# Optimization experiments

Hardware: AMD Instinct MI355X
Metric: run time of the kernel (lower is better)

The kernel has to match this reference:

```python
import jax, jax.numpy as jnp
import numpy as np

N, K, D = 32768, 8192, 64

def setup_inputs() -> dict:
    key = jax.random.key(0)
    kx, kc = jax.random.split(key)
    x = jax.random.normal(kx, (N, D), dtype=jnp.float32)
    codebook = jax.random.normal(kc, (K, D), dtype=jnp.float32)
    return {"x": x, "codebook": codebook}

def reference(x, codebook):
    # Faithful to: argmin(((codebook[None] - x[:, None])**2).sum(-1), -1)
    # Computed via the expanded squared distance to avoid the [N, K, D]
    # constant per row and does not affect argmin, but we include it so the
    # distance matrix matches the original math exactly.
    x_sq = jnp.sum(x * x, axis=-1, keepdims=True)          # [N, 1]
    c_sq = jnp.sum(codebook * codebook, axis=-1)           # [K]
    cross = jnp.einsum('nd,kd->nk', x, codebook)           # [N, K]
    dists = x_sq - 2.0 * cross + c_sq[None, :]             # [N, K]
    return jnp.argmin(dists, axis=-1)                      # [N] int32
```

## Files before the change

### kernel.cpp

```cpp
#include <hip/hip_runtime.h>
#include <math.h>


typedef __attribute__((ext_vector_type(8)))  _Float16 h8v;
typedef __attribute__((ext_vector_type(16))) float f16v;

constexpr int NROWS = 32768;
constexpr int KC    = 8192;
constexpr int DD    = 64;
constexpr int TPB   = 256;
constexpr int PTPB  = 256;
constexpr int BROWS = 64;
constexpr int GUNIT = 4224;
constexpr int NBODY = 64;

__device__ __forceinline__ void split2h(float v, _Float16& h1, _Float16& h2) {
  const float av = fabsf(v);
  _Float16 a = (_Float16)v;
  if (av < 6.1035156e-5f) a = (_Float16)0.f;
  h1 = a;
  h2 = (_Float16)((v - (float)a) * 4096.f);
}

__device__ __forceinline__ void gload_lds16(const void* g, void* l) {
  __builtin_amdgcn_global_load_lds(
      (const __attribute__((address_space(1))) void*)g,
      (__attribute__((address_space(3))) void*)l, 16, 0, 0);
}
__device__ __forceinline__ void gload_lds4(const void* g, void* l) {
  __builtin_amdgcn_global_load_lds(
      (const __attribute__((address_space(1))) void*)g,
      (__attribute__((address_space(3))) void*)l, 4, 0, 0);
}

__device__ __forceinline__ unsigned fkey(float f) {
  const unsigned u = __float_as_uint(f);
  return u ^ (((unsigned)((int)u >> 31)) | 0x80000000u);
}

__global__ void vq_pre_kernel(const float* __restrict__ cb,
                              _Float16* __restrict__ bSwz) {
  const int gidx = blockIdx.x * PTPB + threadIdx.x;
  const int code = gidx >> 2;
  const int kc4  = gidx & 3;
  const float* cp = cb + (size_t)code * DD + kc4 * 16;
  float v[16];
#pragma unroll
  for (int d = 0; d < 16; d += 4) {
    const float4 g = *(const float4*)(cp + d);
    v[d] = g.x; v[d + 1] = g.y; v[d + 2] = g.z; v[d + 3] = g.w;
  }
  float s = 0.f;
#pragma unroll
  for (int d = 0; d < 16; ++d) s = fmaf(v[d], v[d], s);
  s += __shfl_xor(s, 1, 64);
  s += __shfl_xor(s, 2, 64);
  _Float16 p1[16], p2[16];
#pragma unroll
  for (int d = 0; d < 16; ++d) split2h(v[d], p1[d], p2[d]);
  const int g = code >> 5, l = code & 31;
  _Float16* base = bSwz + (size_t)g * GUNIT;
#pragma unroll
  for (int p = 0; p < 2; ++p) {
    const _Float16* pl = p ? p2 : p1;
#pragma unroll
    for (int h = 0; h < 2; ++h) {
      h8v wv;
#pragma unroll
      for (int j = 0; j < 8; ++j) wv[j] = pl[h * 8 + j];
      *(h8v*)(base + (p * 4 + kc4) * 512 + (h * 32 + l) * 8) = wv;
    }
  }
  if (kc4 == 0) {
    float* cs2 = (float*)(base + 4096);
    cs2[l] = s; cs2[32 + l] = s;
  }
}

__global__ __launch_bounds__(TPB, 2)
void vq_mfma_kernel(const float* __restrict__ x, const _Float16* __restrict__ bSwz,
                    int* __restrict__ out) {
  __shared__ alignas(16) _Float16 ldsBf[2 * 4 * GUNIT];
  __shared__ alignas(16) unsigned long long ldsRed[BROWS][4];

  const int tid  = threadIdx.x;
  const int lane = tid & 63;
  const int w    = tid >> 6;
  const int half = lane >> 5;
  const int col  = lane & 31;
  const int blockRow = blockIdx.x * BROWS;

  _Float16* ldsA = ldsBf;
  {
    const int row = tid >> 2, dseg = (tid & 3) * 16;
    const float* xp = x + (size_t)(blockRow + row) * DD + dseg;
    float v[16];
#pragma unroll
    for (int d = 0; d < 16; d += 4) {
      const float4 g = *(const float4*)(xp + d);
      v[d] = g.x; v[d + 1] = g.y; v[d + 2] = g.z; v[d + 3] = g.w;
    }
    _Float16 qa[16], qb[16];
#pragma unroll
    for (int e = 0; e < 16; ++e) split2h(v[e], qa[e], qb[e]);
#pragma unroll
    for (int h2 = 0; h2 < 2; ++h2) {
      h8v a, b;
#pragma unroll
      for (int j = 0; j < 8; ++j) { a[j] = qa[h2 * 8 + j]; b[j] = qb[h2 * 8 + j]; }
      const int slot = (tid & 3) * 2 + h2;
      *(h8v*)&ldsA[(0 * 64 + row) * 64 + (slot ^ (row & 7)) * 8] = a;
      *(h8v*)&ldsA[(1 * 64 + row) * 64 + (slot ^ (row & 7)) * 8] = b;
    }
  }
  asm volatile("s_waitcnt lgkmcnt(0)\n\ts_barrier" ::: "memory");

  h8v afr[2][2][4];
#pragma unroll
  for (int q = 0; q < 2; ++q)
#pragma unroll
    for (int p = 0; p < 2; ++p)
#pragma unroll
      for (int kc = 0; kc < 4; ++kc) {
        const int arow = q * 32 + col;
        const int slot = kc * 2 + half;
        afr[q][p][kc] =
            *(const h8v*)&ldsA[(p * 64 + arow) * 64 + ((slot ^ (arow & 7))) * 8];
      }
  asm volatile("s_waitcnt lgkmcnt(0)\n\ts_barrier" ::: "memory");

  {
    const _Float16* gs = bSwz + (size_t)w * GUNIT;
    _Float16* ld = ldsBf + w * GUNIT;
#pragma unroll
    for (int c = 0; c < 8; ++c)
      gload_lds16(gs + c * 512 + lane * 8, ld + c * 512 + lane * 8);
    gload_lds4((const float*)(gs + 4096) + lane, (float*)(ld + 4096));
  }

  float bestD[32];
  unsigned bestC[32];
  float distP[32];
#pragma unroll
  for (int i = 0; i < 32; ++i) {
    bestD[i] = INFINITY; bestC[i] = 0u; distP[i] = INFINITY;
  }
  unsigned codeP = 0u;

  const f16v Z = {0.f,0.f,0.f,0.f,0.f,0.f,0.f,0.f,0.f,0.f,0.f,0.f,0.f,0.f,0.f,0.f};

  for (int t = 0; t < NBODY; ++t) {
    asm volatile("s_waitcnt vmcnt(0)" ::: "memory");
    if (t + 1 < NBODY) {
      const _Float16* gs = bSwz + (size_t)((t + 1) * 4 + w) * GUNIT;
      _Float16* ld = ldsBf + ((t + 1) & 1) * (4 * GUNIT) + w * GUNIT;
#pragma unroll
      for (int c = 0; c < 8; ++c)
        gload_lds16(gs + c * 512 + lane * 8, ld + c * 512 + lane * 8);
      gload_lds4((const float*)(gs + 4096) + lane, (float*)(ld + 4096));
    }
    const _Float16* rb = ldsBf + (t & 1) * (4 * GUNIT) + w * GUNIT;
    h8v b0[4], b1[4];
#pragma unroll
    for (int kc = 0; kc < 4; ++kc) {
      b0[kc] = *(const h8v*)(rb + kc * 512 + lane * 8);
      b1[kc] = *(const h8v*)(rb + (4 + kc) * 512 + lane * 8);
    }
    const float cs = ((const float*)(rb + 4096))[lane];

#pragma unroll
    for (int i = 0; i < 32; ++i)
      if (distP[i] < bestD[i]) { bestD[i] = distP[i]; bestC[i] = codeP; }

    __builtin_amdgcn_s_setprio(1);
    f16v A0 = Z, B0v = Z, A1 = Z, B1v = Z;
#pragma unroll
    for (int kc = 0; kc < 4; ++kc) {
      A0  = __builtin_amdgcn_mfma_f32_32x32x16_f16(afr[0][0][kc], b0[kc], A0,  0, 0, 0);
      A1  = __builtin_amdgcn_mfma_f32_32x32x16_f16(afr[1][0][kc], b0[kc], A1,  0, 0, 0);
      B0v = __builtin_amdgcn_mfma_f32_32x32x16_f16(afr[0][0][kc], b1[kc], B0v, 0, 0, 0);
      B1v = __builtin_amdgcn_mfma_f32_32x32x16_f16(afr[1][0][kc], b1[kc], B1v, 0, 0, 0);
    }
#pragma unroll
    for (int kc = 0; kc < 4; ++kc) {
      B0v = __builtin_amdgcn_mfma_f32_32x32x16_f16(afr[0][1][kc], b0[kc], B0v, 0, 0, 0);
      B1v = __builtin_amdgcn_mfma_f32_32x32x16_f16(afr[1][1][kc], b0[kc], B1v, 0, 0, 0);
    }
    __builtin_amdgcn_s_setprio(0);

#pragma unroll
    for (int i = 0; i < 16; ++i) {
      distP[i]      = fmaf(-2.f, fmaf(B0v[i], 2.44140625e-4f, A0[i]), cs);
      distP[16 + i] = fmaf(-2.f, fmaf(B1v[i], 2.44140625e-4f, A1[i]), cs);
    }
    codeP = (unsigned)((t * 4 + w) * 32 + col);
  }
#pragma unroll
  for (int i = 0; i < 32; ++i)
    if (distP[i] < bestD[i]) { bestD[i] = distP[i]; bestC[i] = codeP; }

  unsigned long long key[32];
#pragma unroll
  for (int i = 0; i < 32; ++i)
    key[i] = ((unsigned long long)fkey(bestD[i]) << 32) | bestC[i];
#pragma unroll
  for (int i = 0; i < 32; ++i) {
#pragma unroll
    for (int m = 1; m < 32; m <<= 1) {
      const unsigned long long o = __shfl_xor(key[i], m, 64);
      if (o < key[i]) key[i] = o;
    }
  }
  if (col == 0) {
#pragma unroll
    for (int i = 0; i < 32; ++i) {
      const int ii = i & 15, q = i >> 4;
      const int row = q * 32 + (ii & 3) + 8 * (ii >> 2) + 4 * half;
      ldsRed[row][w] = key[i];
    }
  }
  __syncthreads();
  if (tid < BROWS) {
    unsigned long long a = ldsRed[tid][0];
    const unsigned long long b = ldsRed[tid][1];
    const unsigned long long c = ldsRed[tid][2];
    const unsigned long long d = ldsRed[tid][3];
    if (b < a) a = b;
    if (c < a) a = c;
    if (d < a) a = d;
    out[blockRow + tid] = (int)(unsigned)(a & 0xFFFFFFFFull);
  }
}

extern "C" void kernel_launch(void* const* d_in, const int* in_sizes, int n_in,
                              void* d_out, int out_size, void* d_ws, size_t ws_size,
                              hipStream_t stream) {
  const float* x  = (const float*)d_in[0];
  const float* cb = (const float*)d_in[1];
  int* out = (int*)d_out;

  _Float16* bSwz = (_Float16*)d_ws;

  vq_pre_kernel<<<dim3(KC * 4 / PTPB), dim3(PTPB), 0, stream>>>(cb, bSwz);
  vq_mfma_kernel<<<dim3(NROWS / BROWS), dim3(TPB), 0, stream>>>(x, bSwz, out);
}
```

Before: 179.0 us.

## Load codebook fragments directly to registers with double-buffered prefetch, drop LDS staging

Replaces the global-to-LDS async staging of codebook tiles with direct global loads into VGPRs, double-buffered in registers via a 2x-unrolled loop that prefetches the next tile during the current MFMA body. The software-pipelined deferred argmin update (distP/codeP) is removed in favour of an immediate compare after each tile. This cuts LDS traffic, the vmcnt waits and the LDS footprint. In exchange it raises register pressure and exposes global-load latency directly to the waves.

Result: slower. 235.4 us (+31.5%).

```diff
diff --git a/kernel.cpp b/kernel.cpp
--- a/kernel.cpp
+++ b/kernel.cpp
@@ -22,17 +22,6 @@
   h2 = (_Float16)((v - (float)a) * 4096.f);
 }
 
-__device__ __forceinline__ void gload_lds16(const void* g, void* l) {
-  __builtin_amdgcn_global_load_lds(
-      (const __attribute__((address_space(1))) void*)g,
-      (__attribute__((address_space(3))) void*)l, 16, 0, 0);
-}
-__device__ __forceinline__ void gload_lds4(const void* g, void* l) {
-  __builtin_amdgcn_global_load_lds(
-      (const __attribute__((address_space(1))) void*)g,
-      (__attribute__((address_space(3))) void*)l, 4, 0, 0);
-}
-
 __device__ __forceinline__ unsigned fkey(float f) {
   const unsigned u = __float_as_uint(f);
   return u ^ (((unsigned)((int)u >> 31)) | 0x80000000u);
@@ -77,10 +66,49 @@
   }
 }
 
+#define LOADB(P0, P1, CS, T)                                                  \
+  {                                                                           \
+    const _Float16* gs = bSwz + (size_t)((T) * 4 + w) * GUNIT + lane * 8;     \
+    _Pragma("unroll")                                                         \
+    for (int kc = 0; kc < 4; ++kc) {                                          \
+      P0[kc] = *(const h8v*)(gs + kc * 512);                                  \
+      P1[kc] = *(const h8v*)(gs + (4 + kc) * 512);                            \
+    }                                                                         \
+    CS = *(const float*)((const char*)(bSwz + (size_t)((T) * 4 + w) * GUNIT   \
+                                       + 4096) + lane * 4);                   \
+  }
+
+#define BODY(P0, P1, CS, T)                                                   \
+  {                                                                           \
+    __builtin_amdgcn_s_setprio(1);                                            \
+    f16v A0 = Z, B0v = Z, A1 = Z, B1v = Z;                                    \
+    _Pragma("unroll")                                                         \
+    for (int kc = 0; kc < 4; ++kc) {                                          \
+      A0  = __builtin_amdgcn_mfma_f32_32x32x16_f16(afr[0][0][kc], P0[kc], A0,  0, 0, 0); \
+      A1  = __builtin_amdgcn_mfma_f32_32x32x16_f16(afr[1][0][kc], P0[kc], A1,  0, 0, 0); \
+      B0v = __builtin_amdgcn_mfma_f32_32x32x16_f16(afr[0][0][kc], P1[kc], B0v, 0, 0, 0); \
+      B1v = __builtin_amdgcn_mfma_f32_32x32x16_f16(afr[1][0][kc], P1[kc], B1v, 0, 0, 0); \
+    }                                                                         \
+    _Pragma("unroll")                                                         \
+    for (int kc = 0; kc < 4; ++kc) {                                          \
+      B0v = __builtin_amdgcn_mfma_f32_32x32x16_f16(afr[0][1][kc], P0[kc], B0v, 0, 0, 0); \
+      B1v = __builtin_amdgcn_mfma_f32_32x32x16_f16(afr[1][1][kc], P0[kc], B1v, 0, 0, 0); \
+    }                                                                         \
+    __builtin_amdgcn_s_setprio(0);                                            \
+    const unsigned code = (unsigned)(((T) * 4 + w) * 32 + col);               \
+    _Pragma("unroll")                                                         \
+    for (int i = 0; i < 16; ++i) {                                            \
+      const float d0 = fmaf(-2.f, fmaf(B0v[i], 2.44140625e-4f, A0[i]), CS);   \
+      if (d0 < bestD[i])      { bestD[i] = d0;      bestC[i] = code; }        \
+      const float d1 = fmaf(-2.f, fmaf(B1v[i], 2.44140625e-4f, A1[i]), CS);   \
+      if (d1 < bestD[16 + i]) { bestD[16 + i] = d1; bestC[16 + i] = code; }   \
+    }                                                                         \
+  }
+
 __global__ __launch_bounds__(TPB, 2)
 void vq_mfma_kernel(const float* __restrict__ x, const _Float16* __restrict__ bSwz,
                     int* __restrict__ out) {
-  __shared__ alignas(16) _Float16 ldsBf[2 * 4 * GUNIT];
+  __shared__ alignas(16) _Float16 ldsA[2 * BROWS * DD];
   __shared__ alignas(16) unsigned long long ldsRed[BROWS][4];
 
   const int tid  = threadIdx.x;
@@ -90,7 +118,6 @@
   const int col  = lane & 31;
   const int blockRow = blockIdx.x * BROWS;
 
-  _Float16* ldsA = ldsBf;
   {
     const int row = tid >> 2, dseg = (tid & 3) * 16;
     const float* xp = x + (size_t)(blockRow + row) * DD + dseg;
@@ -113,7 +140,7 @@
       *(h8v*)&ldsA[(1 * 64 + row) * 64 + (slot ^ (row & 7)) * 8] = b;
     }
   }
-  asm volatile("s_waitcnt lgkmcnt(0)\n\ts_barrier" ::: "memory");
+  __syncthreads();
 
   h8v afr[2][2][4];
 #pragma unroll
@@ -127,77 +154,24 @@
         afr[q][p][kc] =
             *(const h8v*)&ldsA[(p * 64 + arow) * 64 + ((slot ^ (arow & 7))) * 8];
       }
-  asm volatile("s_waitcnt lgkmcnt(0)\n\ts_barrier" ::: "memory");
-
-  {
-    const _Float16* gs = bSwz + (size_t)w * GUNIT;
-    _Float16* ld = ldsBf + w * GUNIT;
-#pragma unroll
-    for (int c = 0; c < 8; ++c)
-      gload_lds16(gs + c * 512 + lane * 8, ld + c * 512 + lane * 8);
-    gload_lds4((const float*)(gs + 4096) + lane, (float*)(ld + 4096));
-  }
 
   float bestD[32];
   unsigned bestC[32];
-  float distP[32];
-#pragma unroll
-  for (int i = 0; i < 32; ++i) {
-    bestD[i] = INFINITY; bestC[i] = 0u; distP[i] = INFINITY;
-  }
-  unsigned codeP = 0u;
+#pragma unroll
+  for (int i = 0; i < 32; ++i) { bestD[i] = INFINITY; bestC[i] = 0u; }
 
   const f16v Z = {0.f,0.f,0.f,0.f,0.f,0.f,0.f,0.f,0.f,0.f,0.f,0.f,0.f,0.f,0.f,0.f};
 
-  for (int t = 0; t < NBODY; ++t) {
-    asm volatile("s_waitcnt vmcnt(0)" ::: "memory");
-    if (t + 1 < NBODY) {
-      const _Float16* gs = bSwz + (size_t)((t + 1) * 4 + w) * GUNIT;
-      _Float16* ld = ldsBf + ((t + 1) & 1) * (4 * GUNIT) + w * GUNIT;
-#pragma unroll
-      for (int c = 0; c < 8; ++c)
-        gload_lds16(gs + c * 512 + lane * 8, ld + c * 512 + lane * 8);
-      gload_lds4((const float*)(gs + 4096) + lane, (float*)(ld + 4096));
-    }
-    const _Float16* rb = ldsBf + (t & 1) * (4 * GUNIT) + w * GUNIT;
-    h8v b0[4], b1[4];
-#pragma unroll
-    for (int kc = 0; kc < 4; ++kc) {
-      b0[kc] = *(const h8v*)(rb + kc * 512 + lane * 8);
-      b1[kc] = *(const h8v*)(rb + (4 + kc) * 512 + lane * 8);
-    }
-    const float cs = ((const float*)(rb + 4096))[lane];
-
-#pragma unroll
-    for (int i = 0; i < 32; ++i)
-      if (distP[i] < bestD[i]) { bestD[i] = distP[i]; bestC[i] = codeP; }
-
-    __builtin_amdgcn_s_setprio(1);
-    f16v A0 = Z, B0v = Z, A1 = Z, B1v = Z;
-#pragma unroll
-    for (int kc = 0; kc < 4; ++kc) {
-      A0  = __builtin_amdgcn_mfma_f32_32x32x16_f16(afr[0][0][kc], b0[kc], A0,  0, 0, 0);
-      A1  = __builtin_amdgcn_mfma_f32_32x32x16_f16(afr[1][0][kc], b0[kc], A1,  0, 0, 0);
-      B0v = __builtin_amdgcn_mfma_f32_32x32x16_f16(afr[0][0][kc], b1[kc], B0v, 0, 0, 0);
-      B1v = __builtin_amdgcn_mfma_f32_32x32x16_f16(afr[1][0][kc], b1[kc], B1v, 0, 0, 0);
-    }
-#pragma unroll
-    for (int kc = 0; kc < 4; ++kc) {
-      B0v = __builtin_amdgcn_mfma_f32_32x32x16_f16(afr[0][1][kc], b0[kc], B0v, 0, 0, 0);
-      B1v = __builtin_amdgcn_mfma_f32_32x32x16_f16(afr[1][1][kc], b0[kc], B1v, 0, 0, 0);
-    }
-    __builtin_amdgcn_s_setprio(0);
-
-#pragma unroll
-    for (int i = 0; i < 16; ++i) {
-      distP[i]      = fmaf(-2.f, fmaf(B0v[i], 2.44140625e-4f, A0[i]), cs);
-      distP[16 + i] = fmaf(-2.f, fmaf(B1v[i], 2.44140625e-4f, A1[i]), cs);
-    }
-    codeP = (unsigned)((t * 4 + w) * 32 + col);
-  }
-#pragma unroll
-  for (int i = 0; i < 32; ++i)
-    if (distP[i] < bestD[i]) { bestD[i] = distP[i]; bestC[i] = codeP; }
+  h8v bA0[4], bA1[4]; float csA;
+  h8v bB0[4], bB1[4]; float csB;
+  LOADB(bA0, bA1, csA, 0);
+#pragma unroll 1
+  for (int t = 0; t < NBODY; t += 2) {
+    LOADB(bB0, bB1, csB, t + 1);
+    BODY(bA0, bA1, csA, t);
+    if (t + 2 < NBODY) LOADB(bA0, bA1, csA, t + 2);
+    BODY(bB0, bB1, csB, t + 1);
+  }
 
   unsigned long long key[32];
 #pragma unroll
```
